# Kernel optimization log

Measured on AMD Instinct MI355X. Metric: run time of the kernel, lower is better.

## Reference

```python
import jax, jax.numpy as jnp
import numpy as np

NEG_SLOPE = 0.2  # PyG GATConv default LeakyReLU slope
BN_EPS = 1e-5


def gat_layer(x, src, dst, W, a_src, a_dst, num_nodes):
    """PyG-style GATConv (no dropout, eval mode). Returns [N, H, C]."""
    H, C = a_src.shape
    h = (x @ W).reshape(-1, H, C)                       # [N,H,C]
    s_src = jnp.einsum('nhc,hc->nh', h, a_src)          # [N,H]
    s_dst = jnp.einsum('nhc,hc->nh', h, a_dst)          # [N,H]
    e = jax.nn.leaky_relu(s_src[src] + s_dst[dst], NEG_SLOPE)  # [E,H]
    # segment softmax over incoming edges of each dst node
    e_max = jax.ops.segment_max(e, dst, num_segments=num_nodes)  # [N,H]
    e_exp = jnp.exp(e - e_max[dst])
    denom = jax.ops.segment_sum(e_exp, dst, num_segments=num_nodes)
    alpha = e_exp / (denom[dst] + 1e-16)                # [E,H]
    msg = h[src] * alpha[:, :, None]                    # [E,H,C] (dominant intermediate)
    return jax.ops.segment_sum(msg, dst, num_segments=num_nodes)  # [N,H,C]


def setup_inputs() -> dict:
    key = jax.random.key(0)
    ks = jax.random.split(key, 12)
    N, Din, Hdim, Heads, Dout = 50000, 128, 128, 8, 128
    E = 150000
    inp = {}
    inp['x'] = jax.random.normal(ks[0], (N, Din), dtype=jnp.float32)
    inp['edge_index'] = jax.random.randint(ks[1], (2, E), 0, N, dtype=jnp.int64)
    sc1 = 1.0 / np.sqrt(Din)
    inp['W1'] = jax.random.uniform(ks[2], (Din, Heads * Hdim), minval=-sc1, maxval=sc1, dtype=jnp.float32)
    inp['a_src1'] = jax.random.normal(ks[3], (Heads, Hdim), dtype=jnp.float32) * 0.1
    inp['a_dst1'] = jax.random.normal(ks[4], (Heads, Hdim), dtype=jnp.float32) * 0.1
    inp['b1'] = jnp.zeros((Heads * Hdim,), dtype=jnp.float32)
    inp['gamma'] = jnp.ones((Heads * Hdim,), dtype=jnp.float32)
    inp['beta'] = jnp.zeros((Heads * Hdim,), dtype=jnp.float32)
    sc2 = 1.0 / np.sqrt(Heads * Hdim)
    inp['W2'] = jax.random.uniform(ks[5], (Heads * Hdim, Dout), minval=-sc2, maxval=sc2, dtype=jnp.float32)
    inp['a_src2'] = jax.random.normal(ks[6], (1, Dout), dtype=jnp.float32) * 0.1
    inp['a_dst2'] = jax.random.normal(ks[7], (1, Dout), dtype=jnp.float32) * 0.1
    inp['b2'] = jnp.zeros((Dout,), dtype=jnp.float32)
    return inp


def reference(x, W1, a_src1, a_dst1, b1, gamma, beta, W2, a_src2, a_dst2, b2, edge_index):
    N = x.shape[0]
    src, dst = edge_index[0], edge_index[1]
    # GAT layer 1: heads=8, concat=True
    h1 = gat_layer(x, src, dst, W1, a_src1, a_dst1, N)   # [N,8,128]
    h1 = h1.reshape(N, -1) + b1                          # [N,1024]
    # BatchNorm1d (training-mode batch stats, biased variance as in torch)
    mu = jnp.mean(h1, axis=0)
    var = jnp.var(h1, axis=0)
    h1 = gamma * (h1 - mu) * jax.lax.rsqrt(var + BN_EPS) + beta
    h1 = jax.nn.elu(h1)
    # GAT layer 2: heads=1, concat=False (mean == squeeze for 1 head)
    h2 = gat_layer(h1, src, dst, W2, a_src2, a_dst2, N)  # [N,1,128]
    return h2[:, 0, :] + b2
```

## Files before the change

kernel.cpp:

```cpp
#include <hip/hip_runtime.h>
#include <hip/hip_bf16.h>
#include <math.h>

#define NEG_SLOPE 0.2f
#define BN_EPS 1e-5f

typedef short bf16x8 __attribute__((ext_vector_type(8)));
typedef float f32x4 __attribute__((ext_vector_type(4)));

__device__ __forceinline__ float bf2f(unsigned short u) {
  union { unsigned int i; float f; } v;
  v.i = ((unsigned int)u) << 16;
  return v.f;
}
__device__ __forceinline__ unsigned short f2bf(float f) {
  union { unsigned int i; float f; } v;
  v.f = f;
  unsigned int i = v.i;
  unsigned int r = (i + 0x7fffu + ((i >> 16) & 1u)) >> 16;
  return (unsigned short)r;
}

__global__ __launch_bounds__(256) void detect_kernel(
    const unsigned int* __restrict__ xw, const unsigned int* __restrict__ eiw,
    int E, int* __restrict__ flags) {
  __shared__ int cnt[2];
  if (threadIdx.x < 2) cnt[threadIdx.x] = 0;
  __syncthreads();
  int t = threadIdx.x;
  int inrange = 0;
  for (int i = t; i < 2048; i += 256) {
    unsigned int e = (xw[i] >> 7) & 0xFFu;
    inrange += (e >= 100u && e <= 135u) ? 1 : 0;
  }
  atomicAdd(&cnt[0], inrange);
  int M = min(1024, E / 2);
  int zeros = 0;
  for (int i = t; i < M; i += 256) zeros += (eiw[2 * i + 1] == 0u) ? 1 : 0;
  atomicAdd(&cnt[1], zeros);
  __syncthreads();
  if (t == 0) {
    flags[0] = (cnt[0] > 1536) ? 1 : 0;
    flags[1] = (cnt[1] > M / 2) ? 1 : 0;
  }
}

__global__ __launch_bounds__(256) void canon_w_t(
    const void* __restrict__ src, unsigned short* __restrict__ dst, int Kdim,
    int Ndim, const int* __restrict__ flags) {
  int i = blockIdx.x * 256 + threadIdx.x;
  if (i >= Kdim * Ndim) return;
  int k = i / Ndim, n = i - k * Ndim;
  unsigned short v = flags[0] ? ((const unsigned short*)src)[i]
                              : f2bf(((const float*)src)[i]);
  dst[(size_t)n * Kdim + k] = v;
}

__global__ __launch_bounds__(1024) void canon_params(
    const void* s0, const void* s1, const void* s2, const void* s3,
    const void* s4, const void* s5, const void* s6, const void* s7,
    unsigned short* d0, unsigned short* d1, unsigned short* d2,
    unsigned short* d3, unsigned short* d4, unsigned short* d5,
    unsigned short* d6, unsigned short* d7, const int* __restrict__ flags) {
  int b = blockIdx.x, t = threadIdx.x;
  const void* s;
  unsigned short* d;
  int n;
  switch (b) {
    case 0: s = s0; d = d0; n = 1024; break;
    case 1: s = s1; d = d1; n = 1024; break;
    case 2: s = s2; d = d2; n = 1024; break;
    case 3: s = s3; d = d3; n = 1024; break;
    case 4: s = s4; d = d4; n = 1024; break;
    case 5: s = s5; d = d5; n = 128; break;
    case 6: s = s6; d = d6; n = 128; break;
    default: s = s7; d = d7; n = 128; break;
  }
  if (t < n)
    d[t] = flags[0] ? ((const unsigned short*)s)[t]
                    : f2bf(((const float*)s)[t]);
}

__global__ __launch_bounds__(256) void canon_idx(
    const int* __restrict__ ei, int* __restrict__ eis, int* __restrict__ eid,
    int E, const int* __restrict__ flags) {
  int e = blockIdx.x * 256 + threadIdx.x;
  if (e >= E) return;
  if (flags[1]) {
    eis[e] = ei[2 * (size_t)e];
    eid[e] = ei[2 * (size_t)E + 2 * (size_t)e];
  } else {
    eis[e] = ei[e];
    eid[e] = ei[E + e];
  }
}

__global__ __launch_bounds__(256) void gemm1_fused(
    const void* __restrict__ Araw,
    const unsigned short* __restrict__ Bt,
    unsigned short* __restrict__ C,
    const unsigned short* __restrict__ aScr,
    const unsigned short* __restrict__ aDcr,
    float* __restrict__ ssrc,
    float* __restrict__ sdst,
    int N, int MP, const int* __restrict__ flags) {
  __shared__ unsigned short As[64 * 128];
  __shared__ unsigned short Bs[128 * 128];
  __shared__ float sAll[64][8];
  __shared__ float dAll[64][8];

  const int tid = threadIdx.x;
  const int wid = tid >> 6;
  const int lane = tid & 63;
  const int q = lane >> 4;
  const int r = lane & 15;
  const int wm = wid * 16;
  const int m0 = blockIdx.x * 64;

  const int arow = tid >> 4;
  const int ag = tid & 15;

  const int isbf = flags[0];

  bf16x8 ra[4], rb[8];
#pragma unroll
  for (int j = 0; j < 4; ++j) {
    int row = m0 + j * 16 + arow;
    union { bf16x8 v; unsigned short u[8]; } t;
    if (row < N) {
      if (isbf) {
        t.v = *(const bf16x8*)((const unsigned short*)Araw +
                               (size_t)row * 128 + ag * 8);
      } else {
        const float4* f =
            (const float4*)((const float*)Araw + (size_t)row * 128 + ag * 8);
        float4 f0 = f[0];
        float4 f1 = f[1];
        t.u[0] = f2bf(f0.x); t.u[1] = f2bf(f0.y);
        t.u[2] = f2bf(f0.z); t.u[3] = f2bf(f0.w);
        t.u[4] = f2bf(f1.x); t.u[5] = f2bf(f1.y);
        t.u[6] = f2bf(f1.z); t.u[7] = f2bf(f1.w);
      }
    } else {
#pragma unroll
      for (int jj = 0; jj < 8; ++jj) t.u[jj] = 0;
    }
    ra[j] = t.v;
  }
#pragma unroll
  for (int j = 0; j < 8; ++j)
    rb[j] = *(const bf16x8*)(Bt + (size_t)(j * 16 + arow) * 128 + ag * 8);
#pragma unroll
  for (int j = 0; j < 4; ++j) {
    int row = j * 16 + arow;
    int gs = ag ^ (row & 15);
    *(bf16x8*)(As + row * 128 + gs * 8) = ra[j];
  }
#pragma unroll
  for (int j = 0; j < 8; ++j) {
    int row = j * 16 + arow;
    int gs = ag ^ (row & 15);
    *(bf16x8*)(Bs + row * 128 + gs * 8) = rb[j];
  }
  __syncthreads();

  for (int p = 0; p < 8; ++p) {
    if (p < 7) {
#pragma unroll
      for (int j = 0; j < 8; ++j)
        rb[j] = *(const bf16x8*)(Bt +
                 (size_t)((p + 1) * 128 + j * 16 + arow) * 128 + ag * 8);
    }
    f32x4 acc[8] = {};
#pragma unroll
    for (int ks = 0; ks < 4; ++ks) {
      bf16x8 af = *(const bf16x8*)(As + (wm + r) * 128 +
                                   (((ks * 4 + q) ^ r) << 3));
#pragma unroll
      for (int ni = 0; ni < 8; ++ni) {
        bf16x8 bf = *(const bf16x8*)(Bs + (ni * 16 + r) * 128 +
                                     (((ks * 4 + q) ^ r) << 3));
        acc[ni] = __builtin_amdgcn_mfma_f32_16x16x32_bf16(af, bf, acc[ni],
                                                          0, 0, 0);
      }
    }
#pragma unroll
    for (int ni = 0; ni < 8; ++ni)
#pragma unroll
      for (int i = 0; i < 4; ++i)
        C[(size_t)(m0 + wm + q * 4 + i) * 1024 + p * 128 + ni * 16 + r] =
            f2bf(acc[ni][i]);
    float aSv[8], aDv[8];
#pragma unroll
    for (int ni = 0; ni < 8; ++ni) {
      aSv[ni] = bf2f(aScr[p * 128 + ni * 16 + r]);
      aDv[ni] = bf2f(aDcr[p * 128 + ni * 16 + r]);
    }
#pragma unroll
    for (int i = 0; i < 4; ++i) {
      float ps = 0.f, pd = 0.f;
#pragma unroll
      for (int ni = 0; ni < 8; ++ni) {
        ps += acc[ni][i] * aSv[ni];
        pd += acc[ni][i] * aDv[ni];
      }
      ps += __shfl_xor(ps, 1, 64); pd += __shfl_xor(pd, 1, 64);
      ps += __shfl_xor(ps, 2, 64); pd += __shfl_xor(pd, 2, 64);
      ps += __shfl_xor(ps, 4, 64); pd += __shfl_xor(pd, 4, 64);
      ps += __shfl_xor(ps, 8, 64); pd += __shfl_xor(pd, 8, 64);
      if (r == 0) {
        sAll[wm + q * 4 + i][p] = ps;
        dAll[wm + q * 4 + i][p] = pd;
      }
    }
    __syncthreads();
    if (p < 7) {
#pragma unroll
      for (int j = 0; j < 8; ++j) {
        int row = j * 16 + arow;
        int gs = ag ^ (row & 15);
        *(bf16x8*)(Bs + row * 128 + gs * 8) = rb[j];
      }
      __syncthreads();
    }
  }
  __syncthreads();
  if (tid < 128) {
    float4 v = *((const float4*)&sAll[0][0] + tid);
    *((float4*)(ssrc + (size_t)m0 * 8) + tid) = v;
  } else {
    float4 v = *((const float4*)&dAll[0][0] + (tid - 128));
    *((float4*)(sdst + (size_t)m0 * 8) + (tid - 128)) = v;
  }
}

__global__ __launch_bounds__(256) void gemm2_bn(
    const unsigned short* __restrict__ A,
    const unsigned short* __restrict__ Bt,
    float* __restrict__ C,
    const float* __restrict__ scale, const float* __restrict__ shift,
    const unsigned short* __restrict__ aScr,
    const unsigned short* __restrict__ aDcr,
    float* __restrict__ ssrc, float* __restrict__ sdst) {
  constexpr int K = 1024;
  constexpr int BK = 64;
  constexpr int LDA = BK + 8;
  __shared__ unsigned short As[64 * LDA];
  __shared__ unsigned short Bs[128 * LDA];
  __shared__ float sS[2][64];
  __shared__ float sD[2][64];

  const int m0 = blockIdx.x * 64;
  const int tid = threadIdx.x;
  const int wid = tid >> 6;
  const int lane = tid & 63;
  const int q = lane >> 4;
  const int r = lane & 15;
  const int wm = (wid >> 1) * 32;
  const int wn = (wid & 1) * 64;

  f32x4 acc[2][4] = {};

  const int row0 = tid >> 3;
  const int col0 = (tid & 7) * 8;

  bf16x8 ra[2], rb[4];
#pragma unroll
  for (int ca = 0; ca < 2; ++ca)
    ra[ca] = *(const bf16x8*)(A + (size_t)(m0 + row0 + ca * 32) * K + col0);
#pragma unroll
  for (int cb = 0; cb < 4; ++cb)
    rb[cb] = *(const bf16x8*)(Bt + (size_t)(row0 + cb * 32) * K + col0);

  for (int k0 = 0; k0 < K; k0 += BK) {
    float scv[8], shv[8];
    *(float4*)&scv[0] = *(const float4*)(scale + k0 + col0);
    *(float4*)&scv[4] = *(const float4*)(scale + k0 + col0 + 4);
    *(float4*)&shv[0] = *(const float4*)(shift + k0 + col0);
    *(float4*)&shv[4] = *(const float4*)(shift + k0 + col0 + 4);
#pragma unroll
    for (int ca = 0; ca < 2; ++ca) {
      union { bf16x8 v; unsigned short u[8]; } pk;
      pk.v = ra[ca];
#pragma unroll
      for (int j = 0; j < 8; ++j) {
        float f = bf2f(pk.u[j]) * scv[j] + shv[j];
        f = f > 0.f ? f : (__expf(f) - 1.0f);
        pk.u[j] = f2bf(f);
      }
      *(bf16x8*)(&As[(row0 + ca * 32) * LDA + col0]) = pk.v;
    }
#pragma unroll
    for (int cb = 0; cb < 4; ++cb)
      *(bf16x8*)(&Bs[(row0 + cb * 32) * LDA + col0]) = rb[cb];
    __syncthreads();

    int k1 = k0 + BK;
    if (k1 < K) {
#pragma unroll
      for (int ca = 0; ca < 2; ++ca)
        ra[ca] = *(const bf16x8*)(A + (size_t)(m0 + row0 + ca * 32) * K + k1 +
                                  col0);
#pragma unroll
      for (int cb = 0; cb < 4; ++cb)
        rb[cb] = *(const bf16x8*)(Bt + (size_t)(row0 + cb * 32) * K + k1 +
                                  col0);
    }

#pragma unroll
    for (int ks = 0; ks < BK; ks += 32) {
      bf16x8 af[2], bfv[4];
#pragma unroll
      for (int mi = 0; mi < 2; ++mi)
        af[mi] = *(const bf16x8*)(&As[(wm + mi * 16 + r) * LDA + ks + q * 8]);
#pragma unroll
      for (int ni = 0; ni < 4; ++ni)
        bfv[ni] = *(const bf16x8*)(&Bs[(wn + ni * 16 + r) * LDA + ks + q * 8]);
#pragma unroll
      for (int mi = 0; mi < 2; ++mi)
#pragma unroll
        for (int ni = 0; ni < 4; ++ni)
          acc[mi][ni] = __builtin_amdgcn_mfma_f32_16x16x32_bf16(
              af[mi], bfv[ni], acc[mi][ni], 0, 0, 0);
    }
    __syncthreads();
  }

#pragma unroll
  for (int mi = 0; mi < 2; ++mi)
#pragma unroll
    for (int ni = 0; ni < 4; ++ni)
#pragma unroll
      for (int i = 0; i < 4; ++i) {
        int row = m0 + wm + mi * 16 + q * 4 + i;
        int col = wn + ni * 16 + r;
        C[(size_t)row * 128 + col] = acc[mi][ni][i];
      }

  const int half = wid & 1;
  float aSv[4], aDv[4];
#pragma unroll
  for (int ni = 0; ni < 4; ++ni) {
    aSv[ni] = bf2f(aScr[wn + ni * 16 + r]);
    aDv[ni] = bf2f(aDcr[wn + ni * 16 + r]);
  }
#pragma unroll
  for (int mi = 0; mi < 2; ++mi) {
#pragma unroll
    for (int i = 0; i < 4; ++i) {
      float ps = 0.f, pd = 0.f;
#pragma unroll
      for (int ni = 0; ni < 4; ++ni) {
        float v = acc[mi][ni][i];
        ps += v * aSv[ni];
        pd += v * aDv[ni];
      }
      ps += __shfl_xor(ps, 1, 64); pd += __shfl_xor(pd, 1, 64);
      ps += __shfl_xor(ps, 2, 64); pd += __shfl_xor(pd, 2, 64);
      ps += __shfl_xor(ps, 4, 64); pd += __shfl_xor(pd, 4, 64);
      ps += __shfl_xor(ps, 8, 64); pd += __shfl_xor(pd, 8, 64);
      if (r == 0) {
        int rl = wm + mi * 16 + q * 4 + i;
        sS[half][rl] = ps;
        sD[half][rl] = pd;
      }
    }
  }
  __syncthreads();
  if (tid < 64) {
    ssrc[m0 + tid] = sS[0][tid] + sS[1][tid];
    sdst[m0 + tid] = sD[0][tid] + sD[1][tid];
  }
}

__global__ __launch_bounds__(256) void count_dst(const int* __restrict__ eid,
                                                 int E, int* __restrict__ cnt) {
  int e = blockIdx.x * 256 + threadIdx.x;
  if (e < E) atomicAdd(&cnt[eid[e]], 1);
}

__global__ __launch_bounds__(256) void scan_p1(const int* __restrict__ cnt,
                                               int* __restrict__ bsum, int N) {
  __shared__ int sd[256];
  int b = blockIdx.x, t = threadIdx.x;
  int base = b * 2048;
  int s = 0;
  for (int i = t; i < 2048; i += 256) {
    int idx = base + i;
    if (idx < N) s += cnt[idx];
  }
  sd[t] = s;
  __syncthreads();
  for (int o = 128; o > 0; o >>= 1) {
    if (t < o) sd[t] += sd[t + o];
    __syncthreads();
  }
  if (t == 0) bsum[b] = sd[0];
}

__global__ __launch_bounds__(256) void scan_p2(int* __restrict__ bsum, int nb) {
  __shared__ int sd[256];
  int t = threadIdx.x;
  int own = (t < nb) ? bsum[t] : 0;
  sd[t] = own;
  __syncthreads();
  for (int o = 1; o < 256; o <<= 1) {
    int v = (t >= o) ? sd[t - o] : 0;
    __syncthreads();
    sd[t] += v;
    __syncthreads();
  }
  if (t < nb) bsum[t] = sd[t] - own;
}

__global__ __launch_bounds__(256) void scan_p3(
    const int* __restrict__ cnt, const int* __restrict__ bsum,
    int* __restrict__ offsets, int* __restrict__ cursor, int N) {
  __shared__ int sd[256];
  int b = blockIdx.x, t = threadIdx.x;
  int base = b * 2048 + t * 8;
  int c[8];
  int ts = 0;
#pragma unroll
  for (int j = 0; j < 8; ++j) {
    int idx = base + j;
    c[j] = (idx < N) ? cnt[idx] : 0;
    ts += c[j];
  }
  sd[t] = ts;
  __syncthreads();
  for (int o = 1; o < 256; o <<= 1) {
    int v = (t >= o) ? sd[t - o] : 0;
    __syncthreads();
    sd[t] += v;
    __syncthreads();
  }
  int run = bsum[b] + sd[t] - ts;
#pragma unroll
  for (int j = 0; j < 8; ++j) {
    int idx = base + j;
    if (idx < N) {
      offsets[idx] = run;
      cursor[idx] = run;
      run += c[j];
    }
  }
  if (b == gridDim.x - 1 && t == 255) offsets[N] = bsum[b] + sd[255];
}

__global__ __launch_bounds__(256) void scatter_src(
    const int* __restrict__ eis, const int* __restrict__ eid, int E,
    int* __restrict__ cursor, int* __restrict__ srcs) {
  int e = blockIdx.x * 256 + threadIdx.x;
  if (e >= E) return;
  int d = eid[e];
  int pos = atomicAdd(&cursor[d], 1);
  srcs[pos] = eis[e];
}

__global__ __launch_bounds__(256) void agg1_csr(
    const int* __restrict__ offsets, const int* __restrict__ srcs,
    const unsigned short* __restrict__ h1, const float* __restrict__ ssrc,
    const float* __restrict__ sdst, const unsigned short* __restrict__ b1,
    unsigned short* __restrict__ h1n, int N) {
  int n = blockIdx.x * 4 + (threadIdx.x >> 6);
  if (n >= N) return;
  int lane = threadIdx.x & 63;
  int c0 = lane * 8;
  int c1 = 512 + c0;
  int hA = lane >> 4;
  int beg = offsets[n], end = offsets[n + 1];
  float sdA = sdst[n * 8 + hA];
  float sdB = sdst[n * 8 + hA + 4];
  float accA[8] = {}, accB[8] = {};
  float wsA = 0.f, wsB = 0.f;
  int p = beg;
  for (; p + 2 <= end; p += 2) {
    int s0 = srcs[p], s1 = srcs[p + 1];
    float vA0 = ssrc[s0 * 8 + hA] + sdA;
    float vB0 = ssrc[s0 * 8 + hA + 4] + sdB;
    float vA1 = ssrc[s1 * 8 + hA] + sdA;
    float vB1 = ssrc[s1 * 8 + hA + 4] + sdB;
    union { bf16x8 v; unsigned short u[8]; } uA0, uB0, uA1, uB1;
    uA0.v = *(const bf16x8*)(h1 + (size_t)s0 * 1024 + c0);
    uB0.v = *(const bf16x8*)(h1 + (size_t)s0 * 1024 + c1);
    uA1.v = *(const bf16x8*)(h1 + (size_t)s1 * 1024 + c0);
    uB1.v = *(const bf16x8*)(h1 + (size_t)s1 * 1024 + c1);
    vA0 = vA0 > 0.f ? vA0 : NEG_SLOPE * vA0;
    vB0 = vB0 > 0.f ? vB0 : NEG_SLOPE * vB0;
    vA1 = vA1 > 0.f ? vA1 : NEG_SLOPE * vA1;
    vB1 = vB1 > 0.f ? vB1 : NEG_SLOPE * vB1;
    float wA0 = __expf(vA0), wB0 = __expf(vB0);
    float wA1 = __expf(vA1), wB1 = __expf(vB1);
    wsA += wA0 + wA1;
    wsB += wB0 + wB1;
#pragma unroll
    for (int j = 0; j < 8; ++j) {
      accA[j] = fmaf(bf2f(uA0.u[j]), wA0, accA[j]);
      accB[j] = fmaf(bf2f(uB0.u[j]), wB0, accB[j]);
      accA[j] = fmaf(bf2f(uA1.u[j]), wA1, accA[j]);
      accB[j] = fmaf(bf2f(uB1.u[j]), wB1, accB[j]);
    }
  }
  if (p < end) {
    int s0 = srcs[p];
    float vA0 = ssrc[s0 * 8 + hA] + sdA;
    float vB0 = ssrc[s0 * 8 + hA + 4] + sdB;
    union { bf16x8 v; unsigned short u[8]; } uA0, uB0;
    uA0.v = *(const bf16x8*)(h1 + (size_t)s0 * 1024 + c0);
    uB0.v = *(const bf16x8*)(h1 + (size_t)s0 * 1024 + c1);
    vA0 = vA0 > 0.f ? vA0 : NEG_SLOPE * vA0;
    vB0 = vB0 > 0.f ? vB0 : NEG_SLOPE * vB0;
    float wA0 = __expf(vA0), wB0 = __expf(vB0);
    wsA += wA0;
    wsB += wB0;
#pragma unroll
    for (int j = 0; j < 8; ++j) {
      accA[j] = fmaf(bf2f(uA0.u[j]), wA0, accA[j]);
      accB[j] = fmaf(bf2f(uB0.u[j]), wB0, accB[j]);
    }
  }
  float invA = 1.0f / (wsA + 1e-16f);
  float invB = 1.0f / (wsB + 1e-16f);
  union { bf16x8 v; unsigned short u[8]; } bA, bB, oA, oB;
  bA.v = *(const bf16x8*)(b1 + c0);
  bB.v = *(const bf16x8*)(b1 + c1);
#pragma unroll
  for (int j = 0; j < 8; ++j) {
    oA.u[j] = f2bf(accA[j] * invA + bf2f(bA.u[j]));
    oB.u[j] = f2bf(accB[j] * invB + bf2f(bB.u[j]));
  }
  *(bf16x8*)(h1n + (size_t)n * 1024 + c0) = oA.v;
  *(bf16x8*)(h1n + (size_t)n * 1024 + c1) = oB.v;
}

__global__ __launch_bounds__(256) void bn_stats_part(
    const unsigned short* __restrict__ h1n, float* __restrict__ part, int N,
    int rowsPerBlock) {
  int b = blockIdx.x;
  int half = threadIdx.x >> 7;
  int t = threadIdx.x & 127;
  int c = t * 8;
  int r0 = b * rowsPerBlock;
  int r1 = min(r0 + rowsPerBlock, N);
  float s[8] = {0, 0, 0, 0, 0, 0, 0, 0};
  float q[8] = {0, 0, 0, 0, 0, 0, 0, 0};
  int r = r0 + half;
  for (; r + 2 < r1; r += 4) {
    union { bf16x8 v; unsigned short u[8]; } u0, u1;
    u0.v = *(const bf16x8*)(h1n + (size_t)r * 1024 + c);
    u1.v = *(const bf16x8*)(h1n + (size_t)(r + 2) * 1024 + c);
#pragma unroll
    for (int j = 0; j < 8; ++j) {
      float v0 = bf2f(u0.u[j]);
      float v1 = bf2f(u1.u[j]);
      s[j] += v0 + v1;
      q[j] = fmaf(v0, v0, q[j]);
      q[j] = fmaf(v1, v1, q[j]);
    }
  }
  for (; r < r1; r += 2) {
    union { bf16x8 v; unsigned short u[8]; } u0;
    u0.v = *(const bf16x8*)(h1n + (size_t)r * 1024 + c);
#pragma unroll
    for (int j = 0; j < 8; ++j) {
      float v0 = bf2f(u0.u[j]);
      s[j] += v0;
      q[j] = fmaf(v0, v0, q[j]);
    }
  }
  float* pb = part + ((size_t)b * 2 + half) * 2048;
#pragma unroll
  for (int j = 0; j < 8; ++j) {
    pb[c + j] = s[j];
    pb[1024 + c + j] = q[j];
  }
}

__global__ __launch_bounds__(256) void bn_reduce_finalize(
    const float* __restrict__ part, int nparts,
    const unsigned short* __restrict__ gamma,
    const unsigned short* __restrict__ beta, float* __restrict__ scale,
    float* __restrict__ shift, int N) {
  int c = blockIdx.x * 4 + (threadIdx.x >> 6);
  int lane = threadIdx.x & 63;
  float s = 0.f, q = 0.f;
  for (int b = lane; b < nparts; b += 64) {
    s += part[(size_t)b * 2048 + c];
    q += part[(size_t)b * 2048 + 1024 + c];
  }
#pragma unroll
  for (int o = 32; o > 0; o >>= 1) {
    s += __shfl_xor(s, o, 64);
    q += __shfl_xor(q, o, 64);
  }
  if (lane == 0) {
    float inv_n = 1.0f / (float)N;
    float mu = s * inv_n;
    float var = q * inv_n - mu * mu;
    float sc = bf2f(gamma[c]) * rsqrtf(var + BN_EPS);
    scale[c] = sc;
    shift[c] = bf2f(beta[c]) - mu * sc;
  }
}

__global__ __launch_bounds__(256) void agg2_csr(
    const int* __restrict__ offsets, const int* __restrict__ srcs,
    const float* __restrict__ h2, const float* __restrict__ ssrc,
    const float* __restrict__ sdst, const unsigned short* __restrict__ b2,
    void* __restrict__ out, const int* __restrict__ flags, int N) {
  int n = blockIdx.x * 4 + (threadIdx.x >> 6);
  if (n >= N) return;
  int c = (threadIdx.x & 63) * 2;
  int beg = offsets[n], end = offsets[n + 1];
  float sd = sdst[n];
  float a0 = 0.f, a1 = 0.f, wsum = 0.f;
  int p = beg;
  for (; p + 2 <= end; p += 2) {
    int s0 = srcs[p], s1 = srcs[p + 1];
    float v0 = ssrc[s0] + sd;
    float v1 = ssrc[s1] + sd;
    float2 u0 = *(const float2*)(h2 + (size_t)s0 * 128 + c);
    float2 u1 = *(const float2*)(h2 + (size_t)s1 * 128 + c);
    v0 = v0 > 0.f ? v0 : NEG_SLOPE * v0;
    v1 = v1 > 0.f ? v1 : NEG_SLOPE * v1;
    float w0 = __expf(v0), w1 = __expf(v1);
    wsum += w0 + w1;
    a0 = fmaf(u0.x, w0, a0);
    a1 = fmaf(u0.y, w0, a1);
    a0 = fmaf(u1.x, w1, a0);
    a1 = fmaf(u1.y, w1, a1);
  }
  if (p < end) {
    int s0 = srcs[p];
    float v0 = ssrc[s0] + sd;
    float2 u0 = *(const float2*)(h2 + (size_t)s0 * 128 + c);
    v0 = v0 > 0.f ? v0 : NEG_SLOPE * v0;
    float w0 = __expf(v0);
    wsum += w0;
    a0 = fmaf(u0.x, w0, a0);
    a1 = fmaf(u0.y, w0, a1);
  }
  float inv = 1.0f / (wsum + 1e-16f);
  unsigned int bb = *(const unsigned int*)(b2 + c);
  float r0 = a0 * inv + bf2f(bb & 0xffff);
  float r1 = a1 * inv + bf2f(bb >> 16);
  if (flags[0]) {
    unsigned int o = (unsigned int)f2bf(r0) | ((unsigned int)f2bf(r1) << 16);
    *(unsigned int*)((unsigned short*)out + (size_t)n * 128 + c) = o;
  } else {
    *(float2*)((float*)out + (size_t)n * 128 + c) = make_float2(r0, r1);
  }
}

extern "C" void kernel_launch(void* const* d_in, const int* in_sizes, int n_in,
                              void* d_out, int out_size, void* d_ws,
                              size_t ws_size, hipStream_t stream) {
  const void* x      = d_in[0];
  const int*  ei     = (const int*)d_in[1];
  const void* W1     = d_in[2];
  const void* a_src1 = d_in[3];
  const void* a_dst1 = d_in[4];
  const void* b1     = d_in[5];
  const void* gamma  = d_in[6];
  const void* beta   = d_in[7];
  const void* W2     = d_in[8];
  const void* a_src2 = d_in[9];
  const void* a_dst2 = d_in[10];
  const void* b2     = d_in[11];

  const int N = in_sizes[0] / 128;
  const int E = in_sizes[1] / 2;
  const int MP = ((N + 127) / 128) * 128;
  const int NB = (N + 2047) / 2048;
  const int NSTAT = 512;
  const int RPB = (N + NSTAT - 1) / NSTAT;

  char* ws = (char*)d_ws;
  size_t off = 0;
  unsigned short* h1  = (unsigned short*)(ws + off); off += (size_t)MP * 1024 * 2;
  char* h1n_base = ws + off;
  unsigned short* h1n = (unsigned short*)h1n_base;   off += (size_t)MP * 1024 * 2;
  float* ssrc1 = (float*)(ws + off); off += (size_t)MP * 8 * 4;
  float* sdst1 = (float*)(ws + off); off += (size_t)MP * 8 * 4;
  int* offsets = (int*)(ws + off); off += ((size_t)(N + 1) * 4 + 63) & ~63ull;
  int* srcs    = (int*)(ws + off); off += (size_t)E * 4;
  float* part  = (float*)(ws + off); off += (size_t)NSTAT * 2 * 2048 * 4;
  unsigned short* W1t = (unsigned short*)(ws + off); off += 131072 * 2;
  unsigned short* W2t = (unsigned short*)(ws + off); off += 131072 * 2;
  unsigned short* as1c = (unsigned short*)(ws + off); off += 1024 * 2;
  unsigned short* ad1c = (unsigned short*)(ws + off); off += 1024 * 2;
  unsigned short* b1c  = (unsigned short*)(ws + off); off += 1024 * 2;
  unsigned short* gmc  = (unsigned short*)(ws + off); off += 1024 * 2;
  unsigned short* btc  = (unsigned short*)(ws + off); off += 1024 * 2;
  unsigned short* as2c = (unsigned short*)(ws + off); off += 128 * 2;
  unsigned short* ad2c = (unsigned short*)(ws + off); off += 128 * 2;
  unsigned short* b2c  = (unsigned short*)(ws + off); off += 128 * 2;
  float* scale = (float*)(ws + off); off += 1024 * 4;
  float* shift = (float*)(ws + off); off += 1024 * 4;
  int* bsum    = (int*)(ws + off); off += 256 * 4;
  int* flags   = (int*)(ws + off); off += 64;
  int* eis    = (int*)(h1n_base + (16u << 20));
  int* eid    = eis + E;
  int* cnt    = eid + E;
  int* cursor = cnt + N;
  float* h2    = (float*)h1;
  float* ssrc2 = ssrc1;
  float* sdst2 = sdst1;

  detect_kernel<<<1, 256, 0, stream>>>((const unsigned int*)x,
                                       (const unsigned int*)ei, E, flags);
  canon_w_t<<<(131072 + 255) / 256, 256, 0, stream>>>(W1, W1t, 128, 1024, flags);
  canon_w_t<<<(131072 + 255) / 256, 256, 0, stream>>>(W2, W2t, 1024, 128, flags);
  canon_params<<<8, 1024, 0, stream>>>(a_src1, a_dst1, b1, gamma, beta, a_src2,
                                       a_dst2, b2, as1c, ad1c, b1c, gmc, btc,
                                       as2c, ad2c, b2c, flags);
  canon_idx<<<(E + 255) / 256, 256, 0, stream>>>(ei, eis, eid, E, flags);

  hipMemsetAsync(cnt, 0, (size_t)N * 4, stream);
  hipMemsetAsync((char*)h1n + (size_t)N * 1024 * 2, 0,
                 (size_t)(MP - N) * 1024 * 2, stream);

  count_dst<<<(E + 255) / 256, 256, 0, stream>>>(eid, E, cnt);
  scan_p1<<<NB, 256, 0, stream>>>(cnt, bsum, N);
  scan_p2<<<1, 256, 0, stream>>>(bsum, NB);
  scan_p3<<<NB, 256, 0, stream>>>(cnt, bsum, offsets, cursor, N);
  scatter_src<<<(E + 255) / 256, 256, 0, stream>>>(eis, eid, E, cursor, srcs);

  gemm1_fused<<<MP / 64, 256, 0, stream>>>(x, W1t, h1, as1c, ad1c, ssrc1,
                                           sdst1, N, MP, flags);
  agg1_csr<<<(N + 3) / 4, 256, 0, stream>>>(offsets, srcs, h1, ssrc1, sdst1,
                                            b1c, h1n, N);

  bn_stats_part<<<NSTAT, 256, 0, stream>>>(h1n, part, N, RPB);
  bn_reduce_finalize<<<256, 256, 0, stream>>>(part, NSTAT * 2, gmc, btc, scale,
                                              shift, N);

  gemm2_bn<<<MP / 64, 256, 0, stream>>>(h1n, W2t, h2, scale, shift, as2c,
                                        ad2c, ssrc2, sdst2);
  agg2_csr<<<(N + 3) / 4, 256, 0, stream>>>(offsets, srcs, h2, ssrc2, sdst2,
                                            b2c, d_out, flags, N);
}
```

Baseline: 353.8 us.

## Split gemm1 across four column-group blocks with register-resident B fragments

Each gemm1 block now covers 64 rows by 256 output columns instead of all 1024, so the grid is four times larger. Each wave keeps its 64-column slice of W1 in registers, which removes the shared-memory B tile and the per-pass syncthreads. The attention score partials are now reduced per head-pair through a small shared array and written as float2 per column group. The A tile is reloaded and converted four times per row block, and the BN stats partial count drops from 512 to 256.

```diff
diff --git a/kernel.cpp b/kernel.cpp
--- a/kernel.cpp
+++ b/kernel.cpp
@@ -105,102 +105,93 @@
     float* __restrict__ sdst,
     int N, int MP, const int* __restrict__ flags) {
   __shared__ unsigned short As[64 * 128];
-  __shared__ unsigned short Bs[128 * 128];
-  __shared__ float sAll[64][8];
-  __shared__ float dAll[64][8];
+  __shared__ float sP[64][2][2];
+  __shared__ float dP[64][2][2];
 
   const int tid = threadIdx.x;
   const int wid = tid >> 6;
   const int lane = tid & 63;
   const int q = lane >> 4;
   const int r = lane & 15;
-  const int wm = wid * 16;
-  const int m0 = blockIdx.x * 64;
-
-  const int arow = tid >> 4;
-  const int ag = tid & 15;
-
-  const int isbf = flags[0];
-
-  bf16x8 ra[4], rb[8];
-#pragma unroll
-  for (int j = 0; j < 4; ++j) {
-    int row = m0 + j * 16 + arow;
-    union { bf16x8 v; unsigned short u[8]; } t;
-    if (row < N) {
-      if (isbf) {
-        t.v = *(const bf16x8*)((const unsigned short*)Araw +
-                               (size_t)row * 128 + ag * 8);
+  const int bid = blockIdx.x;
+  const int m0 = (bid >> 2) * 64;
+  const int cg = bid & 3;
+  const int n0 = cg * 256 + wid * 64;
+
+  bf16x8 bfr[4][4];
+#pragma unroll
+  for (int ni = 0; ni < 4; ++ni)
+#pragma unroll
+    for (int ks = 0; ks < 4; ++ks)
+      bfr[ni][ks] = *(const bf16x8*)(Bt + (size_t)(n0 + ni * 16 + r) * 128 +
+                                     (ks * 4 + q) * 8);
+
+  {
+    const int arow = tid >> 4, ag = tid & 15;
+    const int isbf = flags[0];
+    union { bf16x8 v; unsigned short u[8]; } t[4];
+#pragma unroll
+    for (int j = 0; j < 4; ++j) {
+      int row = m0 + j * 16 + arow;
+      if (row < N) {
+        if (isbf) {
+          t[j].v = *(const bf16x8*)((const unsigned short*)Araw +
+                                    (size_t)row * 128 + ag * 8);
+        } else {
+          const float4* f =
+              (const float4*)((const float*)Araw + (size_t)row * 128 + ag * 8);
+          float4 f0 = f[0];
+          float4 f1 = f[1];
+          t[j].u[0] = f2bf(f0.x); t[j].u[1] = f2bf(f0.y);
+          t[j].u[2] = f2bf(f0.z); t[j].u[3] = f2bf(f0.w);
+          t[j].u[4] = f2bf(f1.x); t[j].u[5] = f2bf(f1.y);
+          t[j].u[6] = f2bf(f1.z); t[j].u[7] = f2bf(f1.w);
+        }
       } else {
-        const float4* f =
-            (const float4*)((const float*)Araw + (size_t)row * 128 + ag * 8);
-        float4 f0 = f[0];
-        float4 f1 = f[1];
-        t.u[0] = f2bf(f0.x); t.u[1] = f2bf(f0.y);
-        t.u[2] = f2bf(f0.z); t.u[3] = f2bf(f0.w);
-        t.u[4] = f2bf(f1.x); t.u[5] = f2bf(f1.y);
-        t.u[6] = f2bf(f1.z); t.u[7] = f2bf(f1.w);
+#pragma unroll
+        for (int jj = 0; jj < 8; ++jj) t[j].u[jj] = 0;
       }
-    } else {
-#pragma unroll
-      for (int jj = 0; jj < 8; ++jj) t.u[jj] = 0;
-    }
-    ra[j] = t.v;
-  }
-#pragma unroll
-  for (int j = 0; j < 8; ++j)
-    rb[j] = *(const bf16x8*)(Bt + (size_t)(j * 16 + arow) * 128 + ag * 8);
-#pragma unroll
-  for (int j = 0; j < 4; ++j) {
-    int row = j * 16 + arow;
-    int gs = ag ^ (row & 15);
-    *(bf16x8*)(As + row * 128 + gs * 8) = ra[j];
-  }
-#pragma unroll
-  for (int j = 0; j < 8; ++j) {
-    int row = j * 16 + arow;
-    int gs = ag ^ (row & 15);
-    *(bf16x8*)(Bs + row * 128 + gs * 8) = rb[j];
+    }
+#pragma unroll
+    for (int j = 0; j < 4; ++j) {
+      int row = j * 16 + arow;
+      *(bf16x8*)(As + row * 128 + (ag ^ (row & 15)) * 8) = t[j].v;
+    }
   }
   __syncthreads();
 
-  for (int p = 0; p < 8; ++p) {
-    if (p < 7) {
-#pragma unroll
-      for (int j = 0; j < 8; ++j)
-        rb[j] = *(const bf16x8*)(Bt +
-                 (size_t)((p + 1) * 128 + j * 16 + arow) * 128 + ag * 8);
-    }
-    f32x4 acc[8] = {};
-#pragma unroll
-    for (int ks = 0; ks < 4; ++ks) {
-      bf16x8 af = *(const bf16x8*)(As + (wm + r) * 128 +
-                                   (((ks * 4 + q) ^ r) << 3));
-#pragma unroll
-      for (int ni = 0; ni < 8; ++ni) {
-        bf16x8 bf = *(const bf16x8*)(Bs + (ni * 16 + r) * 128 +
-                                     (((ks * 4 + q) ^ r) << 3));
-        acc[ni] = __builtin_amdgcn_mfma_f32_16x16x32_bf16(af, bf, acc[ni],
-                                                          0, 0, 0);
-      }
-    }
-#pragma unroll
-    for (int ni = 0; ni < 8; ++ni)
+  float aSv[4], aDv[4];
+#pragma unroll
+  for (int ni = 0; ni < 4; ++ni) {
+    aSv[ni] = bf2f(aScr[n0 + ni * 16 + r]);
+    aDv[ni] = bf2f(aDcr[n0 + ni * 16 + r]);
+  }
+
+#pragma unroll
+  for (int rg = 0; rg < 4; ++rg) {
+    bf16x8 af[4];
+#pragma unroll
+    for (int ks = 0; ks < 4; ++ks)
+      af[ks] = *(const bf16x8*)(As + (rg * 16 + r) * 128 +
+                                (((ks * 4 + q) ^ r) << 3));
+    f32x4 acc[4] = {};
+#pragma unroll
+    for (int ks = 0; ks < 4; ++ks)
+#pragma unroll
+      for (int ni = 0; ni < 4; ++ni)
+        acc[ni] = __builtin_amdgcn_mfma_f32_16x16x32_bf16(af[ks], bfr[ni][ks],
+                                                          acc[ni], 0, 0, 0);
+#pragma unroll
+    for (int ni = 0; ni < 4; ++ni)
 #pragma unroll
       for (int i = 0; i < 4; ++i)
-        C[(size_t)(m0 + wm + q * 4 + i) * 1024 + p * 128 + ni * 16 + r] =
+        C[(size_t)(m0 + rg * 16 + q * 4 + i) * 1024 + n0 + ni * 16 + r] =
             f2bf(acc[ni][i]);
-    float aSv[8], aDv[8];
-#pragma unroll
-    for (int ni = 0; ni < 8; ++ni) {
-      aSv[ni] = bf2f(aScr[p * 128 + ni * 16 + r]);
-      aDv[ni] = bf2f(aDcr[p * 128 + ni * 16 + r]);
-    }
 #pragma unroll
     for (int i = 0; i < 4; ++i) {
       float ps = 0.f, pd = 0.f;
 #pragma unroll
-      for (int ni = 0; ni < 8; ++ni) {
+      for (int ni = 0; ni < 4; ++ni) {
         ps += acc[ni][i] * aSv[ni];
         pd += acc[ni][i] * aDv[ni];
       }
@@ -209,28 +200,19 @@
       ps += __shfl_xor(ps, 4, 64); pd += __shfl_xor(pd, 4, 64);
       ps += __shfl_xor(ps, 8, 64); pd += __shfl_xor(pd, 8, 64);
       if (r == 0) {
-        sAll[wm + q * 4 + i][p] = ps;
-        dAll[wm + q * 4 + i][p] = pd;
+        sP[rg * 16 + q * 4 + i][wid >> 1][wid & 1] = ps;
+        dP[rg * 16 + q * 4 + i][wid >> 1][wid & 1] = pd;
       }
     }
-    __syncthreads();
-    if (p < 7) {
-#pragma unroll
-      for (int j = 0; j < 8; ++j) {
-        int row = j * 16 + arow;
-        int gs = ag ^ (row & 15);
-        *(bf16x8*)(Bs + row * 128 + gs * 8) = rb[j];
-      }
-      __syncthreads();
-    }
   }
   __syncthreads();
-  if (tid < 128) {
-    float4 v = *((const float4*)&sAll[0][0] + tid);
-    *((float4*)(ssrc + (size_t)m0 * 8) + tid) = v;
-  } else {
-    float4 v = *((const float4*)&dAll[0][0] + (tid - 128));
-    *((float4*)(sdst + (size_t)m0 * 8) + (tid - 128)) = v;
+  if (tid < 64) {
+    float2 s = make_float2(sP[tid][0][0] + sP[tid][0][1],
+                           sP[tid][1][0] + sP[tid][1][1]);
+    float2 d = make_float2(dP[tid][0][0] + dP[tid][0][1],
+                           dP[tid][1][0] + dP[tid][1][1]);
+    *(float2*)(ssrc + (size_t)(m0 + tid) * 8 + cg * 2) = s;
+    *(float2*)(sdst + (size_t)(m0 + tid) * 8 + cg * 2) = d;
   }
 }
 
@@ -673,7 +655,7 @@
   const int E = in_sizes[1] / 2;
   const int MP = ((N + 127) / 128) * 128;
   const int NB = (N + 2047) / 2048;
-  const int NSTAT = 512;
+  const int NSTAT = 256;
   const int RPB = (N + NSTAT - 1) / NSTAT;
 
   char* ws = (char*)d_ws;
@@ -727,8 +709,8 @@
   scan_p3<<<NB, 256, 0, stream>>>(cnt, bsum, offsets, cursor, N);
   scatter_src<<<(E + 255) / 256, 256, 0, stream>>>(eis, eid, E, cursor, srcs);
 
-  gemm1_fused<<<MP / 64, 256, 0, stream>>>(x, W1t, h1, as1c, ad1c, ssrc1,
-                                           sdst1, N, MP, flags);
+  gemm1_fused<<<(MP / 64) * 4, 256, 0, stream>>>(x, W1t, h1, as1c, ad1c,
+                                                 ssrc1, sdst1, N, MP, flags);
   agg1_csr<<<(N + 3) / 4, 256, 0, stream>>>(offsets, srcs, h1, ssrc1, sdst1,
                                             b1c, h1n, N);
 
```

After: 361.5 us. +2.2%, slower.
